# Optimization experiments

Measured on AMD Instinct MI355X. Metric: run time of the kernel, lower is better.

Reference implementation:

```python
import jax, jax.numpy as jnp
import numpy as np

B = 1024
FEAT = 512
C = 2
H = 256
TAU = 5.0
EPS = 1e-8


def setup_inputs() -> dict:
    key = jax.random.key(0)
    ks = jax.random.split(key, 5)
    X_c = jax.random.normal(ks[0], (B, FEAT), dtype=jnp.float32)
    labels_or_logits = jax.random.normal(ks[1], (B, C), dtype=jnp.float32)
    adj = jax.random.normal(ks[2], (B, B), dtype=jnp.float32)
    # MLP params (torch Linear default-ish init scale)
    W1 = jax.random.normal(ks[3], (FEAT + C, H), dtype=jnp.float32) * (1.0 / np.sqrt(FEAT + C))
    b1 = jnp.zeros((H,), dtype=jnp.float32)
    W2 = jax.random.normal(ks[4], (H, 1), dtype=jnp.float32) * (1.0 / np.sqrt(H))
    b2 = jnp.zeros((1,), dtype=jnp.float32)
    return {"X_c": X_c, "labels_or_logits": labels_or_logits, "adj": adj,
            "W1": W1, "b1": b1, "W2": W2, "b2": b2}


def reference(X_c, labels_or_logits, adj, W1, b1, W2, b2):
    # pairwise absolute feature differences: [B, B, FEAT]
    feat_diff = jnp.abs(X_c[:, None, :] - X_c[None, :, :])
    # logits path (2-D input): softmax over classes
    labels_oh = jax.nn.softmax(labels_or_logits, axis=-1)  # [B, C]
    label_sim = labels_oh[:, None, :] * labels_oh[None, :, :]  # [B, B, C]
    # Split first linear across the concat boundary to avoid concat alloc:
    # cat([feat_diff, label_sim]) @ W1 == feat_diff @ W1[:FEAT] + label_sim @ W1[FEAT:]
    h = (jnp.einsum('ijf,fh->ijh', feat_diff, W1[:FEAT]) +
         jnp.einsum('ijc,ch->ijh', label_sim, W1[FEAT:]) + b1)
    h = jax.nn.gelu(h, approximate=False)
    h_scores = jax.nn.sigmoid(jnp.einsum('ijh,ho->ijo', h, W2)[..., 0] + b2[0])  # [B, B]
    adj_refined = jax.nn.softmax(adj + TAU * jnp.log(h_scores + EPS), axis=-1)
    return adj_refined, h_scores
```

## Files before the change

### kernel.cpp

```cpp
#include <hip/hip_runtime.h>
#include <stdint.h>

#define BN   1024
#define FEATN 512
#define HDIM 256
#define TAUF 5.0f
#define EPSF 1e-8f

typedef __attribute__((ext_vector_type(8))) _Float16 half8;
typedef __attribute__((ext_vector_type(4))) float f32x4;

#if defined(__has_builtin)
#if __has_builtin(__builtin_amdgcn_rcpf)
#define HAVE_RCPF 1
#endif
#endif

#ifdef HAVE_RCPF
__device__ __forceinline__ float fast_rcp(float x) { return __builtin_amdgcn_rcpf(x); }
#else
__device__ __forceinline__ float fast_rcp(float x) { return 1.0f / x; }
#endif

__device__ __forceinline__ float gelu_fast(float x) {
  float s = fmaf(x * x, 0.07135481627f, 1.59576912161f) * x;
  float e = __expf(s);
  return x * e * fast_rcp(e + 1.0f);
}

__global__ __launch_bounds__(256) void prep_kernel(const float* __restrict__ W1,
                                                   const float* __restrict__ lg,
                                                   _Float16* __restrict__ w1h,
                                                   float* __restrict__ oh) {
  int b = blockIdx.x, t = threadIdx.x;
  if (b < FEATN) {
    int k = b, n = t;
    w1h[(((k >> 3) * HDIM) + n) * 8 + (k & 7)] = (_Float16)W1[k * HDIM + n];
  } else {
    int i = (b - FEATN) * 256 + t;
    float l0 = lg[2 * i], l1 = lg[2 * i + 1];
    float m = fmaxf(l0, l1);
    float e0 = __expf(l0 - m), e1 = __expf(l1 - m);
    float inv = 1.0f / (e0 + e1);
    oh[2 * i] = e0 * inv;
    oh[2 * i + 1] = e1 * inv;
  }
}

__global__ __launch_bounds__(256, 4) void gemm_kernel(const float* __restrict__ X,
                                                      const _Float16* __restrict__ w1h,
                                                      const float* __restrict__ oh,
                                                      const float* __restrict__ W1,
                                                      const float* __restrict__ b1,
                                                      const float* __restrict__ W2,
                                                      const float* __restrict__ b2,
                                                      float* __restrict__ out_hs) {
  __shared__ __align__(16) _Float16 sX[16 * 520];
  __shared__ __align__(16) half8 sA[2][2][4][64];
  __shared__ float sScore[64 * 4];
  __shared__ float sLab0[64], sLab1[64];

  const int tid = threadIdx.x;
  const int L = tid & 63;
  const int w = tid >> 6;

  int bi = blockIdx.y, bj = blockIdx.x;
  if (bj > bi) { bi = 127 - bi; bj = 128 - bj; }
  const int i0 = bi * 8;
  const int j0 = bj * 8;

  #pragma unroll
  for (int it = 0; it < 4; ++it) {
    int idx = tid + it * 256;
    int row = idx >> 6;
    int oc = idx & 63;
    int grow = (row < 8) ? (i0 + row) : (j0 + row - 8);
    const float* gp = X + grow * FEATN + oc * 8;
    float4 a = *(const float4*)gp;
    float4 c = *(const float4*)(gp + 4);
    half8 hv;
    hv[0] = (_Float16)a.x; hv[1] = (_Float16)a.y; hv[2] = (_Float16)a.z; hv[3] = (_Float16)a.w;
    hv[4] = (_Float16)c.x; hv[5] = (_Float16)c.y; hv[6] = (_Float16)c.z; hv[7] = (_Float16)c.w;
    *(half8*)(sX + row * 520 + oc * 8) = hv;
  }
  if (tid < 64) {
    int gi = i0 + (tid >> 3), gj = j0 + (tid & 7);
    sLab0[tid] = oh[2 * gi] * oh[2 * gj];
    sLab1[tid] = oh[2 * gi + 1] * oh[2 * gj + 1];
  }

  const int nl = L & 15;
  const int koct = L >> 4;
  const _Float16* cxi = sX + (2 * w + (nl >> 3)) * 520 + koct * 8;
  const _Float16* cxj = sX + (8 + (L & 7)) * 520 + koct * 8;

  const _Float16* bbase = w1h + ((koct * HDIM) + w * 64 + nl) * 8;

  f32x4 acc[4][4];
  #pragma unroll
  for (int s = 0; s < 4; ++s)
    #pragma unroll
    for (int u = 0; u < 4; ++u) acc[s][u] = (f32x4){0.f, 0.f, 0.f, 0.f};

  __syncthreads();

  #define CONSTRUCT(kt, buf, st)                                          \
    {                                                                     \
      half8 xi = *(const half8*)(cxi + (kt) * 32);                        \
      half8 xj = *(const half8*)(cxj + (kt) * 32);                        \
      union { half8 h; unsigned u4[4]; } U;                               \
      U.h = xi - xj;                                                      \
      U.u4[0] &= 0x7FFF7FFFu; U.u4[1] &= 0x7FFF7FFFu;                     \
      U.u4[2] &= 0x7FFF7FFFu; U.u4[3] &= 0x7FFF7FFFu;                     \
      sA[buf][st][w][L] = U.h;                                            \
    }

  #define CONSUME(kt, buf, st)                                            \
    {                                                                     \
      half8 afr[4];                                                       \
      _Pragma("unroll")                                                   \
      for (int s = 0; s < 4; ++s) afr[s] = sA[buf][st][s][L];             \
      half8 bfr[4];                                                       \
      _Pragma("unroll")                                                   \
      for (int u = 0; u < 4; ++u)                                         \
        bfr[u] = *(const half8*)(bbase + (kt) * 8192 + u * 128);          \
      _Pragma("unroll")                                                   \
      for (int s = 0; s < 4; ++s)                                         \
        _Pragma("unroll")                                                 \
        for (int u = 0; u < 4; ++u)                                       \
          acc[s][u] = __builtin_amdgcn_mfma_f32_16x16x32_f16(             \
              afr[s], bfr[u], acc[s][u], 0, 0, 0);                        \
    }

  CONSTRUCT(0, 0, 0)
  CONSTRUCT(1, 0, 1)
  __syncthreads();

  #pragma unroll 2
  for (int t = 0; t < 8; ++t) {
    const int buf = t & 1;
    CONSUME(2 * t, buf, 0)
    CONSUME(2 * t + 1, buf, 1)
    if (t < 7) {
      CONSTRUCT(2 * t + 2, 1 - buf, 0)
      CONSTRUCT(2 * t + 3, 1 - buf, 1)
    }
    __syncthreads();
  }
  #undef CONSTRUCT
  #undef CONSUME

  const int q = L >> 4;
  float w1l0[4], w1l1[4], bb1[4], ww2[4];
  #pragma unroll
  for (int u = 0; u < 4; ++u) {
    int n = w * 64 + u * 16 + nl;
    w1l0[u] = W1[512 * HDIM + n];
    w1l1[u] = W1[513 * HDIM + n];
    bb1[u] = b1[n];
    ww2[u] = W2[n];
  }
  #pragma unroll
  for (int s = 0; s < 4; ++s) {
    #pragma unroll
    for (int r = 0; r < 4; ++r) {
      int m = s * 16 + q * 4 + r;
      float l0v = sLab0[m], l1v = sLab1[m];
      float v = 0.f;
      #pragma unroll
      for (int u = 0; u < 4; ++u) {
        float e = acc[s][u][r] + l0v * w1l0[u] + l1v * w1l1[u] + bb1[u];
        v += gelu_fast(e) * ww2[u];
      }
      v += __shfl_xor(v, 1, 64);
      v += __shfl_xor(v, 2, 64);
      v += __shfl_xor(v, 4, 64);
      v += __shfl_xor(v, 8, 64);
      if (nl == 0) sScore[m * 4 + w] = v;
    }
  }
  __syncthreads();
  if (tid < 64) {
    float s4 = sScore[tid * 4 + 0] + sScore[tid * 4 + 1] + sScore[tid * 4 + 2] +
               sScore[tid * 4 + 3] + b2[0];
    float hsv = fast_rcp(1.0f + __expf(-s4));
    int r = tid >> 3, c = tid & 7;
    out_hs[(size_t)(i0 + r) * BN + (j0 + c)] = hsv;
    if (i0 != j0) {
      float tv = __shfl(hsv, (c << 3) | r, 64);
      out_hs[(size_t)(j0 + r) * BN + (i0 + c)] = tv;
    }
  }
}

__global__ __launch_bounds__(256) void softmax_kernel(const float* __restrict__ adj,
                                                      const float* __restrict__ hs,
                                                      float* __restrict__ out) {
  int i = blockIdx.x, t = threadIdx.x;
  __shared__ float redm[4];
  __shared__ float reds[4];
  float l[4];
  float mx = -1e30f;
  #pragma unroll
  for (int k = 0; k < 4; ++k) {
    int j = t + k * 256;
    float lv = adj[(size_t)i * BN + j] + TAUF * __logf(hs[(size_t)i * BN + j] + EPSF);
    l[k] = lv;
    mx = fmaxf(mx, lv);
  }
  #pragma unroll
  for (int o = 1; o <= 32; o <<= 1) mx = fmaxf(mx, __shfl_xor(mx, o, 64));
  if ((t & 63) == 0) redm[t >> 6] = mx;
  __syncthreads();
  mx = fmaxf(fmaxf(redm[0], redm[1]), fmaxf(redm[2], redm[3]));
  float ex[4];
  float se = 0.f;
  #pragma unroll
  for (int k = 0; k < 4; ++k) { ex[k] = __expf(l[k] - mx); se += ex[k]; }
  #pragma unroll
  for (int o = 1; o <= 32; o <<= 1) se += __shfl_xor(se, o, 64);
  if ((t & 63) == 0) reds[t >> 6] = se;
  __syncthreads();
  se = reds[0] + reds[1] + reds[2] + reds[3];
  float inv = fast_rcp(se);
  #pragma unroll
  for (int k = 0; k < 4; ++k) out[(size_t)i * BN + t + k * 256] = ex[k] * inv;
}

extern "C" void kernel_launch(void* const* d_in, const int* in_sizes, int n_in,
                              void* d_out, int out_size, void* d_ws, size_t ws_size,
                              hipStream_t stream) {
  (void)in_sizes; (void)n_in; (void)out_size; (void)ws_size;
  const float* X   = (const float*)d_in[0];
  const float* lg  = (const float*)d_in[1];
  const float* adj = (const float*)d_in[2];
  const float* W1  = (const float*)d_in[3];
  const float* b1  = (const float*)d_in[4];
  const float* W2  = (const float*)d_in[5];
  const float* b2  = (const float*)d_in[6];
  float* out = (float*)d_out;
  _Float16* w1h = (_Float16*)d_ws;
  float* oh = (float*)((char*)d_ws + FEATN * HDIM * 2);

  float* out_hs = out + (size_t)BN * BN;

  prep_kernel<<<dim3(FEATN + 4), dim3(256), 0, stream>>>(W1, lg, w1h, oh);
  gemm_kernel<<<dim3(65, 128), dim3(256), 0, stream>>>(X, w1h, oh, W1, b1, W2, b2, out_hs);
  softmax_kernel<<<dim3(BN), dim3(256), 0, stream>>>(adj, out_hs, out);
}
```

Baseline: 248.8 us.

## Switch pairwise MLP GEMM to 32x32x16 MFMA tiles with lighter barriers

Replaces the 16x16x32 MFMA tiling with 32x32x16 MFMA instructions, remapping how A fragments from the constructed feature-difference buffer and B fragments of W1 are assigned to lanes and waves, and rewrites the epilogue index mapping and reductions to match. It also swaps __syncthreads for an inline s_waitcnt lgkmcnt(0) plus s_barrier. The aim is fewer MFMA issues and fewer B-fragment loads per output, plus cheaper synchronisation. The risk is that the new lane mapping or the barrier, which waits only on LDS and scalar counters, is subtly wrong.

```diff
diff --git a/kernel.cpp b/kernel.cpp
--- a/kernel.cpp
+++ b/kernel.cpp
@@ -8,7 +8,7 @@
 #define EPSF 1e-8f
 
 typedef __attribute__((ext_vector_type(8))) _Float16 half8;
-typedef __attribute__((ext_vector_type(4))) float f32x4;
+typedef __attribute__((ext_vector_type(16))) float f32x16;
 
 #if defined(__has_builtin)
 #if __has_builtin(__builtin_amdgcn_rcpf)
@@ -27,6 +27,8 @@
   float e = __expf(s);
   return x * e * fast_rcp(e + 1.0f);
 }
+
+#define BAR() asm volatile("s_waitcnt lgkmcnt(0)\n\ts_barrier" ::: "memory")
 
 __global__ __launch_bounds__(256) void prep_kernel(const float* __restrict__ W1,
                                                    const float* __restrict__ lg,
@@ -89,20 +91,22 @@
     sLab1[tid] = oh[2 * gi + 1] * oh[2 * gj + 1];
   }
 
-  const int nl = L & 15;
-  const int koct = L >> 4;
-  const _Float16* cxi = sX + (2 * w + (nl >> 3)) * 520 + koct * 8;
-  const _Float16* cxj = sX + (8 + (L & 7)) * 520 + koct * 8;
-
-  const _Float16* bbase = w1h + ((koct * HDIM) + w * 64 + nl) * 8;
-
-  f32x4 acc[4][4];
-  #pragma unroll
-  for (int s = 0; s < 4; ++s)
+  const int colh = L & 31;
+  const int halfId = L >> 5;
+  const int ms_c = w >> 1;
+  const int kh_c = w & 1;
+  const _Float16* cxi = sX + (4 * ms_c + (colh >> 3)) * 520 + (2 * kh_c + halfId) * 8;
+  const _Float16* cxj = sX + (8 + (L & 7)) * 520 + (2 * kh_c + halfId) * 8;
+
+  const _Float16* blane = w1h + ((halfId * HDIM) + w * 64 + colh) * 8;
+
+  f32x16 acc[2][2];
+  #pragma unroll
+  for (int s = 0; s < 2; ++s)
     #pragma unroll
-    for (int u = 0; u < 4; ++u) acc[s][u] = (f32x4){0.f, 0.f, 0.f, 0.f};
-
-  __syncthreads();
+    for (int u = 0; u < 2; ++u) acc[s][u] = (f32x16){};
+
+  BAR();
 
   #define CONSTRUCT(kt, buf, st)                                          \
     {                                                                     \
@@ -119,22 +123,26 @@
     {                                                                     \
       half8 afr[4];                                                       \
       _Pragma("unroll")                                                   \
-      for (int s = 0; s < 4; ++s) afr[s] = sA[buf][st][s][L];             \
-      half8 bfr[4];                                                       \
+      for (int un = 0; un < 4; ++un) afr[un] = sA[buf][st][un][L];        \
+      half8 bfr[4];                                         \
+      bfr[0] = *(const half8*)(blane + (kt) * 8192 + 0);                  \
+      bfr[1] = *(const half8*)(blane + (kt) * 8192 + 256);                \
+      bfr[2] = *(const half8*)(blane + (kt) * 8192 + 4096);               \
+      bfr[3] = *(const half8*)(blane + (kt) * 8192 + 4096 + 256);         \
       _Pragma("unroll")                                                   \
-      for (int u = 0; u < 4; ++u)                                         \
-        bfr[u] = *(const half8*)(bbase + (kt) * 8192 + u * 128);          \
-      _Pragma("unroll")                                                   \
-      for (int s = 0; s < 4; ++s)                                         \
+      for (int s = 0; s < 2; ++s)                                         \
         _Pragma("unroll")                                                 \
-        for (int u = 0; u < 4; ++u)                                       \
-          acc[s][u] = __builtin_amdgcn_mfma_f32_16x16x32_f16(             \
-              afr[s], bfr[u], acc[s][u], 0, 0, 0);                        \
+        for (int u = 0; u < 2; ++u) {                                     \
+          acc[s][u] = __builtin_amdgcn_mfma_f32_32x32x16_f16(             \
+              afr[2 * s + 0], bfr[u], acc[s][u], 0, 0, 0);                \
+          acc[s][u] = __builtin_amdgcn_mfma_f32_32x32x16_f16(             \
+              afr[2 * s + 1], bfr[2 + u], acc[s][u], 0, 0, 0);            \
+        }                                                                 \
     }
 
   CONSTRUCT(0, 0, 0)
   CONSTRUCT(1, 0, 1)
-  __syncthreads();
+  BAR();
 
   #pragma unroll 2
   for (int t = 0; t < 8; ++t) {
@@ -145,30 +153,29 @@
       CONSTRUCT(2 * t + 2, 1 - buf, 0)
       CONSTRUCT(2 * t + 3, 1 - buf, 1)
     }
-    __syncthreads();
+    BAR();
   }
   #undef CONSTRUCT
   #undef CONSUME
 
-  const int q = L >> 4;
-  float w1l0[4], w1l1[4], bb1[4], ww2[4];
-  #pragma unroll
-  for (int u = 0; u < 4; ++u) {
-    int n = w * 64 + u * 16 + nl;
+  float w1l0[2], w1l1[2], bb1[2], ww2[2];
+  #pragma unroll
+  for (int u = 0; u < 2; ++u) {
+    int n = w * 64 + u * 32 + colh;
     w1l0[u] = W1[512 * HDIM + n];
     w1l1[u] = W1[513 * HDIM + n];
     bb1[u] = b1[n];
     ww2[u] = W2[n];
   }
   #pragma unroll
-  for (int s = 0; s < 4; ++s) {
+  for (int s = 0; s < 2; ++s) {
     #pragma unroll
-    for (int r = 0; r < 4; ++r) {
-      int m = s * 16 + q * 4 + r;
+    for (int r = 0; r < 16; ++r) {
+      int m = s * 32 + (r & 3) + 8 * (r >> 2) + 4 * halfId;
       float l0v = sLab0[m], l1v = sLab1[m];
       float v = 0.f;
       #pragma unroll
-      for (int u = 0; u < 4; ++u) {
+      for (int u = 0; u < 2; ++u) {
         float e = acc[s][u][r] + l0v * w1l0[u] + l1v * w1l1[u] + bb1[u];
         v += gelu_fast(e) * ww2[u];
       }
@@ -176,10 +183,11 @@
       v += __shfl_xor(v, 2, 64);
       v += __shfl_xor(v, 4, 64);
       v += __shfl_xor(v, 8, 64);
-      if (nl == 0) sScore[m * 4 + w] = v;
-    }
-  }
-  __syncthreads();
+      v += __shfl_xor(v, 16, 64);
+      if (colh == 0) sScore[m * 4 + w] = v;
+    }
+  }
+  BAR();
   if (tid < 64) {
     float s4 = sScore[tid * 4 + 0] + sScore[tid * 4 + 1] + sScore[tid * 4 + 2] +
                sScore[tid * 4 + 3] + b2[0];
```

New measurement: 285.1 us. +14.6%, slower.

## Stage X tile in two K halves to cut LDS and raise occupancy

Applied to the files above, without the earlier changes.

Splits the fp16 staging of the 16 input rows into two 256-feature halves, so the shared buffer is half the size. The score scratch now reuses the staging buffer instead of having its own allocation. The K loop is fully unrolled, with a mid-loop restage and an extra barrier. Launch bounds go from 4 to 6 blocks to use the LDS savings for more resident blocks, which tightens the register budget and risks spilling the 64-float accumulators.

```diff
diff --git a/kernel.cpp b/kernel.cpp
--- a/kernel.cpp
+++ b/kernel.cpp
@@ -47,7 +47,7 @@
   }
 }
 
-__global__ __launch_bounds__(256, 4) void gemm_kernel(const float* __restrict__ X,
+__global__ __launch_bounds__(256, 6) void gemm_kernel(const float* __restrict__ X,
                                                       const _Float16* __restrict__ w1h,
                                                       const float* __restrict__ oh,
                                                       const float* __restrict__ W1,
@@ -55,10 +55,10 @@
                                                       const float* __restrict__ W2,
                                                       const float* __restrict__ b2,
                                                       float* __restrict__ out_hs) {
-  __shared__ __align__(16) _Float16 sX[16 * 520];
+  __shared__ __align__(16) _Float16 sXh[16 * 264];
   __shared__ __align__(16) half8 sA[2][2][4][64];
-  __shared__ float sScore[64 * 4];
   __shared__ float sLab0[64], sLab1[64];
+  float* sScore = (float*)sXh;
 
   const int tid = threadIdx.x;
   const int L = tid & 63;
@@ -69,20 +69,27 @@
   const int i0 = bi * 8;
   const int j0 = bj * 8;
 
-  #pragma unroll
-  for (int it = 0; it < 4; ++it) {
-    int idx = tid + it * 256;
-    int row = idx >> 6;
-    int oc = idx & 63;
-    int grow = (row < 8) ? (i0 + row) : (j0 + row - 8);
-    const float* gp = X + grow * FEATN + oc * 8;
-    float4 a = *(const float4*)gp;
-    float4 c = *(const float4*)(gp + 4);
-    half8 hv;
-    hv[0] = (_Float16)a.x; hv[1] = (_Float16)a.y; hv[2] = (_Float16)a.z; hv[3] = (_Float16)a.w;
-    hv[4] = (_Float16)c.x; hv[5] = (_Float16)c.y; hv[6] = (_Float16)c.z; hv[7] = (_Float16)c.w;
-    *(half8*)(sX + row * 520 + oc * 8) = hv;
-  }
+  #define STAGE(h)                                                        \
+    {                                                                     \
+      _Pragma("unroll")                                                   \
+      for (int it = 0; it < 2; ++it) {                                    \
+        int idx = tid + it * 256;       \
+        int row = idx >> 5;                                               \
+        int oc = idx & 31;                                                \
+        int grow = (row < 8) ? (i0 + row) : (j0 + row - 8);               \
+        const float* gp = X + grow * FEATN + (h) * 256 + oc * 8;          \
+        float4 a = *(const float4*)gp;                                    \
+        float4 c = *(const float4*)(gp + 4);                              \
+        half8 hv;                                                         \
+        hv[0] = (_Float16)a.x; hv[1] = (_Float16)a.y;                     \
+        hv[2] = (_Float16)a.z; hv[3] = (_Float16)a.w;                     \
+        hv[4] = (_Float16)c.x; hv[5] = (_Float16)c.y;                     \
+        hv[6] = (_Float16)c.z; hv[7] = (_Float16)c.w;                     \
+        *(half8*)(sXh + row * 264 + oc * 8) = hv;                         \
+      }                                                                   \
+    }
+
+  STAGE(0)
   if (tid < 64) {
     int gi = i0 + (tid >> 3), gj = j0 + (tid & 7);
     sLab0[tid] = oh[2 * gi] * oh[2 * gj];
@@ -91,8 +98,8 @@
 
   const int nl = L & 15;
   const int koct = L >> 4;
-  const _Float16* cxi = sX + (2 * w + (nl >> 3)) * 520 + koct * 8;
-  const _Float16* cxj = sX + (8 + (L & 7)) * 520 + koct * 8;
+  const _Float16* cxi = sXh + (2 * w + (nl >> 3)) * 264 + koct * 8;
+  const _Float16* cxj = sXh + (8 + (L & 7)) * 264 + koct * 8;
 
   const _Float16* bbase = w1h + ((koct * HDIM) + w * 64 + nl) * 8;
 
@@ -104,10 +111,10 @@
 
   __syncthreads();
 
-  #define CONSTRUCT(kt, buf, st)                                          \
+  #define CONSTRUCT(ktl, buf, st)                                         \
     {                                                                     \
-      half8 xi = *(const half8*)(cxi + (kt) * 32);                        \
-      half8 xj = *(const half8*)(cxj + (kt) * 32);                        \
+      half8 xi = *(const half8*)(cxi + (ktl) * 32);                       \
+      half8 xj = *(const half8*)(cxj + (ktl) * 32);                       \
       union { half8 h; unsigned u4[4]; } U;                               \
       U.h = xi - xj;                                                      \
       U.u4[0] &= 0x7FFF7FFFu; U.u4[1] &= 0x7FFF7FFFu;                     \
@@ -136,19 +143,22 @@
   CONSTRUCT(1, 0, 1)
   __syncthreads();
 
-  #pragma unroll 2
-  for (int t = 0; t < 8; ++t) {
-    const int buf = t & 1;
-    CONSUME(2 * t, buf, 0)
-    CONSUME(2 * t + 1, buf, 1)
-    if (t < 7) {
-      CONSTRUCT(2 * t + 2, 1 - buf, 0)
-      CONSTRUCT(2 * t + 3, 1 - buf, 1)
-    }
-    __syncthreads();
-  }
+  CONSUME(0, 0, 0)  CONSUME(1, 0, 1)  CONSTRUCT(2, 1, 0) CONSTRUCT(3, 1, 1) __syncthreads();
+  CONSUME(2, 1, 0)  CONSUME(3, 1, 1)  CONSTRUCT(4, 0, 0) CONSTRUCT(5, 0, 1) __syncthreads();
+  CONSUME(4, 0, 0)  CONSUME(5, 0, 1)  CONSTRUCT(6, 1, 0) CONSTRUCT(7, 1, 1) __syncthreads();
+  STAGE(1)
+  CONSUME(6, 1, 0)  CONSUME(7, 1, 1)
+  __syncthreads();
+  CONSTRUCT(0, 0, 0) CONSTRUCT(1, 0, 1)
+  __syncthreads();
+  CONSUME(8, 0, 0)  CONSUME(9, 0, 1)  CONSTRUCT(2, 1, 0) CONSTRUCT(3, 1, 1) __syncthreads();
+  CONSUME(10, 1, 0) CONSUME(11, 1, 1) CONSTRUCT(4, 0, 0) CONSTRUCT(5, 0, 1) __syncthreads();
+  CONSUME(12, 0, 0) CONSUME(13, 0, 1) CONSTRUCT(6, 1, 0) CONSTRUCT(7, 1, 1) __syncthreads();
+  CONSUME(14, 1, 0) CONSUME(15, 1, 1)
+  __syncthreads();
   #undef CONSTRUCT
   #undef CONSUME
+  #undef STAGE
 
   const int q = L >> 4;
   float w1l0[4], w1l1[4], bb1[4], ww2[4];
```

Result: slower. 823.7 us (+231.1%).
